# Optimization experiments

Measured on AMD Instinct MI355X. Metric: run time of the kernel, lower is better.

Reference implementation:

```python
import jax, jax.numpy as jnp
import numpy as np

B, D_IN, H = 4096, 1024, 2048
TAU_MIN = 0.2
ODE_STEPS = 3


def setup_inputs() -> dict:
    key = jax.random.key(0)
    ks = jax.random.split(key, 10)
    s = lambda k, shape, fan_in: jax.random.normal(k, shape, jnp.float32) / np.sqrt(fan_in)
    return {
        "x": jax.random.normal(ks[0], (B, D_IN), jnp.float32),
        "h": jax.random.normal(ks[1], (B, H), jnp.float32),
        "W_ih": s(ks[2], (H, D_IN), D_IN),
        "b_ih": jnp.zeros((H,), jnp.float32),
        "W_hh": s(ks[3], (H, H), H),
        "b_hh": jnp.zeros((H,), jnp.float32),
        "W_t1": s(ks[4], (H, D_IN + H), D_IN + H),
        "b_t1": jnp.zeros((H,), jnp.float32),
        "W_t2": s(ks[5], (H, H), H),
        "b_t2": jnp.zeros((H,), jnp.float32),
    }


def reference(x, h, W_ih, b_ih, W_hh, b_hh, W_t1, b_t1, W_t2, b_t2):
    # Precompute input-side projections (constant across ODE steps).
    ih = x @ W_ih.T + b_ih  # [B, H]

    def dynamics(h_cur):
        interaction = jnp.tanh(ih + h_cur @ W_hh.T + b_hh)
        z = jnp.concatenate([x, h_cur], axis=-1)  # [B, D_in+H]
        t1 = jax.nn.silu(z @ W_t1.T + b_t1)
        tau = jax.nn.softplus(t1 @ W_t2.T + b_t2) + TAU_MIN
        return (-h_cur + interaction) / tau

    dt = 1.0 / ODE_STEPS
    h_cur = h
    for _ in range(ODE_STEPS):  # RK2 (midpoint) steps
        k1 = dynamics(h_cur)
        h_mid = h_cur + 0.5 * dt * k1
        k2 = dynamics(h_mid)
        h_cur = h_cur + dt * k2
    return h_cur
```

## Files before the change

kernel.cpp:

```cpp
#include <hip/hip_runtime.h>


typedef _Float16 f16;
typedef __attribute__((ext_vector_type(4))) _Float16 f16x4;
typedef __attribute__((ext_vector_type(8))) _Float16 f16x8;
typedef __attribute__((ext_vector_type(4))) float f32x4;

#define TAU_MIN_F 0.2f

__device__ __forceinline__ float rcp_fast(float x) { return __builtin_amdgcn_rcpf(x); }
__device__ __forceinline__ float tanh_fast(float u) {
  float t = __expf(2.0f * u);
  return 1.0f - 2.0f * rcp_fast(t + 1.0f);
}
__device__ __forceinline__ float silu_fast(float u) {
  return u * rcp_fast(1.0f + __expf(-u));
}
__device__ __forceinline__ float softplus_fast(float u) {
  return fmaxf(u, 0.0f) + __logf(1.0f + __expf(-fabsf(u)));
}

__device__ __forceinline__ void glds16(const void* g, void* l) {
  __builtin_amdgcn_global_load_lds(
      (const __attribute__((address_space(1))) unsigned int*)g,
      (__attribute__((address_space(3))) unsigned int*)l,
      16, 0, 0);
}

__global__ void cvt4(const float* __restrict__ s, f16* __restrict__ d, int n4) {
  int i = blockIdx.x * 256 + threadIdx.x;
  if (i >= n4) return;
  float4 v = reinterpret_cast<const float4*>(s)[i];
  f16x4 o = {(_Float16)v.x, (_Float16)v.y, (_Float16)v.z, (_Float16)v.w};
  reinterpret_cast<f16x4*>(d)[i] = o;
}

__global__ void split_wt1(const float* __restrict__ Wt1, f16* __restrict__ Wpre,
                          f16* __restrict__ Wab) {
  int i = blockIdx.x * 256 + threadIdx.x;
  if (i >= 2048 * 768) return;
  int r = i / 768;
  int c4 = (i - r * 768) * 4;
  float4 v = reinterpret_cast<const float4*>(Wt1)[i];
  f16x4 o = {(_Float16)v.x, (_Float16)v.y, (_Float16)v.z, (_Float16)v.w};
  if (c4 < 1024)
    *reinterpret_cast<f16x4*>(Wpre + (size_t)(2048 + r) * 1024 + c4) = o;
  else
    *reinterpret_cast<f16x4*>(Wab + (size_t)(2048 + r) * 2048 + (c4 - 1024)) = o;
}

__global__ void biasprep(const float* __restrict__ bih, const float* __restrict__ bhh,
                         const float* __restrict__ bt1, float* __restrict__ biasp) {
  int i = blockIdx.x * 256 + threadIdx.x;
  if (i >= 4096) return;
  biasp[i] = (i < 2048) ? (bih[i] + bhh[i]) : bt1[i - 2048];
}

__global__ void init_h(const float* __restrict__ h, f16* __restrict__ hb,
                       float* __restrict__ hout) {
  int i = blockIdx.x * 256 + threadIdx.x;
  if (i >= 4096 * 2048 / 4) return;
  float4 v = reinterpret_cast<const float4*>(h)[i];
  reinterpret_cast<float4*>(hout)[i] = v;
  f16x4 o = {(_Float16)v.x, (_Float16)v.y, (_Float16)v.z, (_Float16)v.w};
  reinterpret_cast<f16x4*>(hb)[i] = o;
}

struct EpArgs {
  const float* biasf;
  const f16* pre16;
  const f16* h16;
  f16* out_d;
  f16* out_h;
  const float* bt2;
  const f16* diff;
  const float* h_base;
  float* out_f;
  float coef;
};

template <int EP>
__global__ __launch_bounds__(512, 2)
void gemm256(const f16* __restrict__ A, const f16* __restrict__ Bw,
             int N, int K, EpArgs ep) {
  __shared__ __align__(16) f16 SH[49152];

  const int gx = gridDim.x;
  const int nwg = gx * gridDim.y;
  const int orig = blockIdx.y * gx + blockIdx.x;
  const int cpx = nwg >> 3;
  const int w = (orig & 7) * cpx + (orig >> 3);
  const int bm = (w % gx) * 256;
  const int bn = (w / gx) * 256;

  const int tid = threadIdx.x;
  const int lane = tid & 63;
  const int wid = tid >> 6;
  const int wr = wid >> 2;
  const int wc = wid & 3;

  char* SHb = (char*)SH;

  const int srow = wid * 16 + (lane >> 2);
  const int skof = ((lane & 3) ^ ((lane >> 2) & 3)) << 4;
  const char* Ag0 = (const char*)A + (size_t)(bm + srow) * K * 2 + skof;
  const char* Ag1 = Ag0 + (size_t)128 * K * 2;
  const char* Bg0 = (const char*)Bw + (size_t)(bn + srow) * K * 2 + skof;
  const char* Bg1 = Bg0 + (size_t)128 * K * 2;
  const int dst = wid * 1024;

  const int fr = lane & 15;
  const int rxor = ((lane >> 4) ^ (fr & 3)) << 4;
  const int abase = (wr * 128 + fr) * 64 + rxor;
  const int bbase = 16384 + (wc * 64 + fr) * 64 + rxor;

  f32x4 acc[8][4] = {};
  const int NT = K >> 5;

  auto STAGE_A = [&](int t, int b) {
    const size_t kby = (size_t)t * 64;
    char* base = SHb + b * 32768;
    glds16(Ag0 + kby, base + dst);
    glds16(Ag1 + kby, base + 8192 + dst);
  };
  auto STAGE_B = [&](int t, int b) {
    const size_t kby = (size_t)t * 64;
    char* base = SHb + b * 32768;
    glds16(Bg0 + kby, base + 16384 + dst);
    glds16(Bg1 + kby, base + 24576 + dst);
  };

  STAGE_A(0, 0); STAGE_B(0, 0);
  STAGE_A(1, 1); STAGE_B(1, 1);

  int b = 0;
  for (int t = 0; t < NT - 1; ++t) {
    const int b2 = (b == 0) ? 2 : b - 1;
    asm volatile("s_waitcnt vmcnt(4)" ::: "memory");
    __builtin_amdgcn_s_barrier();
    __builtin_amdgcn_sched_barrier(0);
    const char* bufp = SHb + b * 32768;
    f16x8 af[4], bf[4];
#pragma unroll
    for (int i = 0; i < 4; ++i) af[i] = *reinterpret_cast<const f16x8*>(bufp + abase + i * 1024);
#pragma unroll
    for (int i = 0; i < 4; ++i) bf[i] = *reinterpret_cast<const f16x8*>(bufp + bbase + i * 1024);
    if (t + 2 < NT) STAGE_A(t + 2, b2);
    __builtin_amdgcn_s_barrier();
    __builtin_amdgcn_sched_barrier(0);
    asm volatile("s_waitcnt lgkmcnt(0)" ::: "memory");
    __builtin_amdgcn_sched_barrier(0);
    __builtin_amdgcn_s_setprio(1);
#pragma unroll
    for (int mi = 0; mi < 4; ++mi)
#pragma unroll
      for (int ni = 0; ni < 4; ++ni)
        acc[mi][ni] = __builtin_amdgcn_mfma_f32_16x16x32_f16(af[mi], bf[ni], acc[mi][ni], 0, 0, 0);
    __builtin_amdgcn_s_setprio(0);
    f16x8 ag[4];
#pragma unroll
    for (int i = 0; i < 4; ++i) ag[i] = *reinterpret_cast<const f16x8*>(bufp + abase + (4 + i) * 1024);
    if (t + 2 < NT) STAGE_B(t + 2, b2);
    __builtin_amdgcn_s_barrier();
    __builtin_amdgcn_sched_barrier(0);
    asm volatile("s_waitcnt lgkmcnt(0)" ::: "memory");
    __builtin_amdgcn_sched_barrier(0);
    __builtin_amdgcn_s_setprio(1);
#pragma unroll
    for (int mi = 0; mi < 4; ++mi)
#pragma unroll
      for (int ni = 0; ni < 4; ++ni)
        acc[4 + mi][ni] = __builtin_amdgcn_mfma_f32_16x16x32_f16(ag[mi], bf[ni], acc[4 + mi][ni], 0, 0, 0);
    __builtin_amdgcn_s_setprio(0);
    b = (b == 2) ? 0 : b + 1;
  }
  {
    asm volatile("s_waitcnt vmcnt(0)" ::: "memory");
    __builtin_amdgcn_s_barrier();
    __builtin_amdgcn_sched_barrier(0);
    const char* bufp = SHb + b * 32768;
    f16x8 af[4], bf[4];
#pragma unroll
    for (int i = 0; i < 4; ++i) af[i] = *reinterpret_cast<const f16x8*>(bufp + abase + i * 1024);
#pragma unroll
    for (int i = 0; i < 4; ++i) bf[i] = *reinterpret_cast<const f16x8*>(bufp + bbase + i * 1024);
#pragma unroll
    for (int mi = 0; mi < 4; ++mi)
#pragma unroll
      for (int ni = 0; ni < 4; ++ni)
        acc[mi][ni] = __builtin_amdgcn_mfma_f32_16x16x32_f16(af[mi], bf[ni], acc[mi][ni], 0, 0, 0);
    f16x8 ag[4];
#pragma unroll
    for (int i = 0; i < 4; ++i) ag[i] = *reinterpret_cast<const f16x8*>(bufp + abase + (4 + i) * 1024);
#pragma unroll
    for (int mi = 0; mi < 4; ++mi)
#pragma unroll
      for (int ni = 0; ni < 4; ++ni)
        acc[4 + mi][ni] = __builtin_amdgcn_mfma_f32_16x16x32_f16(ag[mi], bf[ni], acc[4 + mi][ni], 0, 0, 0);
  }
  __syncthreads();

  f16* tb = SH + wid * 1088;
  const int er = (lane >> 4) * 4;
  const int ec = lane & 15;
  const int rr = lane >> 3;
  const int cc = (lane & 7) * 8;
  const int colbase = bn + wc * 64;

#pragma unroll
  for (int mi = 0; mi < 8; ++mi) {
#pragma unroll
    for (int ni = 0; ni < 4; ++ni)
#pragma unroll
      for (int j = 0; j < 4; ++j)
        tb[(er + j) * 68 + ni * 16 + ec] = (f16)acc[mi][ni][j];
#pragma unroll
    for (int it = 0; it < 2; ++it) {
      const int row = rr + it * 8;
      const int gm = bm + wr * 128 + mi * 16 + row;
      const int gn = colbase + cc;
      f16x8 v = *reinterpret_cast<const f16x8*>(tb + row * 68 + cc);
      if constexpr (EP == 0) {
        float4 b0 = *reinterpret_cast<const float4*>(ep.biasf + gn);
        float4 b1 = *reinterpret_cast<const float4*>(ep.biasf + gn + 4);
        f16x8 o;
        o[0] = (f16)((float)v[0] + b0.x); o[1] = (f16)((float)v[1] + b0.y);
        o[2] = (f16)((float)v[2] + b0.z); o[3] = (f16)((float)v[3] + b0.w);
        o[4] = (f16)((float)v[4] + b1.x); o[5] = (f16)((float)v[5] + b1.y);
        o[6] = (f16)((float)v[6] + b1.z); o[7] = (f16)((float)v[7] + b1.w);
        *reinterpret_cast<f16x8*>(ep.out_h + (size_t)gm * N + gn) = o;
      } else {
        f16x8 pr = *reinterpret_cast<const f16x8*>(ep.pre16 + (size_t)gm * 4096 + gn);
        if (colbase < 2048) {
          f16x8 hh = *reinterpret_cast<const f16x8*>(ep.h16 + (size_t)gm * 2048 + gn);
          f16x8 o;
#pragma unroll
          for (int k = 0; k < 8; ++k) {
            float u = (float)v[k] + (float)pr[k];
            o[k] = (f16)(tanh_fast(u) - (float)hh[k]);
          }
          *reinterpret_cast<f16x8*>(ep.out_d + (size_t)gm * 2048 + gn) = o;
        } else {
          f16x8 o;
#pragma unroll
          for (int k = 0; k < 8; ++k) {
            float u = (float)v[k] + (float)pr[k];
            o[k] = (f16)silu_fast(u);
          }
          *reinterpret_cast<f16x8*>(ep.out_h + (size_t)gm * 2048 + (gn - 2048)) = o;
        }
      }
    }
  }
}

template <int EP>
__global__ __launch_bounds__(256)
void gemm_bt(const f16* __restrict__ A, const f16* __restrict__ Bw,
             int M, int N, int K, EpArgs ep) {
  __shared__ __align__(16) f16 SH[8192];

  const int gx = gridDim.x;
  const int nwg = gx * gridDim.y;
  const int orig = blockIdx.y * gx + blockIdx.x;
  const int cpx = nwg >> 3;
  const int w = (orig & 7) * cpx + (orig >> 3);
  const int bm = (w % gx) * 128;
  const int bn = (w / gx) * 128;

  const int tid = threadIdx.x;
  const int lane = tid & 63;
  const int wid = tid >> 6;
  const int wm = (wid >> 1) * 64;
  const int wn = (wid & 1) * 64;

  char* Asb = (char*)SH;
  char* Bsb = (char*)(SH + 4096);

  const int off0 = wid * 2048 + lane * 16;
  const int off1 = off0 + 1024;
  const int row0 = off0 >> 6, cb0 = off0 & 63;
  const int row1 = off1 >> 6, cb1 = off1 & 63;
  const char* Ag0 = (const char*)(A + (size_t)(bm + row0) * K) + cb0;
  const char* Ag1 = (const char*)(A + (size_t)(bm + row1) * K) + cb1;
  const char* Bg0 = (const char*)(Bw + (size_t)(bn + row0) * K) + cb0;
  const char* Bg1 = (const char*)(Bw + (size_t)(bn + row1) * K) + cb1;
  char* ldsA0 = Asb + wid * 2048;
  char* ldsA1 = Asb + wid * 2048 + 1024;
  char* ldsB0 = Bsb + wid * 2048;
  char* ldsB1 = Bsb + wid * 2048 + 1024;

  const int fr = lane & 15;
  const int kb = (lane >> 4) * 16;
  int aoff[4], boff[4];
#pragma unroll
  for (int i = 0; i < 4; ++i) {
    aoff[i] = (wm + i * 16 + fr) * 64 + kb;
    boff[i] = (wn + i * 16 + fr) * 64 + kb;
  }

  f32x4 acc[4][4] = {};
  const int nk = K >> 5;
  for (int kt = 0; kt < nk; ++kt) {
    const size_t kby = (size_t)kt * 64;
    glds16(Ag0 + kby, ldsA0);
    glds16(Ag1 + kby, ldsA1);
    glds16(Bg0 + kby, ldsB0);
    glds16(Bg1 + kby, ldsB1);
    __syncthreads();

    f16x8 af[4], bf[4];
#pragma unroll
    for (int i = 0; i < 4; ++i) af[i] = *reinterpret_cast<const f16x8*>(Asb + aoff[i]);
#pragma unroll
    for (int i = 0; i < 4; ++i) bf[i] = *reinterpret_cast<const f16x8*>(Bsb + boff[i]);

#pragma unroll
    for (int mi = 0; mi < 4; ++mi)
#pragma unroll
      for (int ni = 0; ni < 4; ++ni)
        acc[mi][ni] = __builtin_amdgcn_mfma_f32_16x16x32_f16(af[mi], bf[ni], acc[mi][ni], 0, 0, 0);

    __syncthreads();
  }

  f16* tb = SH + wid * 1088;
  const int er = (lane >> 4) * 4;
  const int ec = lane & 15;
  const int rr = lane >> 3;
  const int cc = (lane & 7) * 8;
  const int colbase = bn + wn;

#pragma unroll
  for (int mi = 0; mi < 4; ++mi) {
#pragma unroll
    for (int ni = 0; ni < 4; ++ni)
#pragma unroll
      for (int j = 0; j < 4; ++j)
        tb[(er + j) * 68 + ni * 16 + ec] = (f16)acc[mi][ni][j];
#pragma unroll
    for (int it = 0; it < 2; ++it) {
      const int row = rr + it * 8;
      const int gm = bm + wm + mi * 16 + row;
      const int gn = colbase + cc;
      f16x8 v = *reinterpret_cast<const f16x8*>(tb + row * 68 + cc);
      const size_t idx = (size_t)gm * 2048 + gn;
      float4 b0 = *reinterpret_cast<const float4*>(ep.bt2 + gn);
      float4 b1 = *reinterpret_cast<const float4*>(ep.bt2 + gn + 4);
      f16x8 df = *reinterpret_cast<const f16x8*>(ep.diff + idx);
      float4 h0 = *reinterpret_cast<const float4*>(ep.h_base + idx);
      float4 h1 = *reinterpret_cast<const float4*>(ep.h_base + idx + 4);
      float bb[8] = {b0.x, b0.y, b0.z, b0.w, b1.x, b1.y, b1.z, b1.w};
      float hb8[8] = {h0.x, h0.y, h0.z, h0.w, h1.x, h1.y, h1.z, h1.w};
      f16x8 o16;
      float on[8];
#pragma unroll
      for (int k = 0; k < 8; ++k) {
        float u = (float)v[k] + bb[k];
        float tau = softplus_fast(u) + TAU_MIN_F;
        float hn = hb8[k] + ep.coef * ((float)df[k] * rcp_fast(tau));
        on[k] = hn;
        o16[k] = (f16)hn;
      }
      *reinterpret_cast<f16x8*>(ep.out_h + idx) = o16;
      if (ep.out_f) {
        float4 o0 = {on[0], on[1], on[2], on[3]};
        float4 o1 = {on[4], on[5], on[6], on[7]};
        *reinterpret_cast<float4*>(ep.out_f + idx) = o0;
        *reinterpret_cast<float4*>(ep.out_f + idx + 4) = o1;
      }
    }
  }
}

extern "C" void kernel_launch(void* const* d_in, const int* in_sizes, int n_in,
                              void* d_out, int out_size, void* d_ws, size_t ws_size,
                              hipStream_t stream) {
  const float* x   = (const float*)d_in[0];
  const float* h   = (const float*)d_in[1];
  const float* Wih = (const float*)d_in[2];
  const float* bih = (const float*)d_in[3];
  const float* Whh = (const float*)d_in[4];
  const float* bhh = (const float*)d_in[5];
  const float* Wt1 = (const float*)d_in[6];
  const float* bt1 = (const float*)d_in[7];
  const float* Wt2 = (const float*)d_in[8];
  const float* bt2 = (const float*)d_in[9];
  float* hout = (float*)d_out;

  char* p = (char*)d_ws;
  auto alloc = [&](size_t bytes) {
    char* r = p;
    p += (bytes + 255) & ~(size_t)255;
    return r;
  };
  f16* xb    = (f16*)alloc((size_t)4096 * 1024 * 2);
  f16* Wpre  = (f16*)alloc((size_t)4096 * 1024 * 2);
  f16* Wab   = (f16*)alloc((size_t)4096 * 2048 * 2);
  f16* Wt2b  = (f16*)alloc((size_t)2048 * 2048 * 2);
  f16* hb    = (f16*)alloc((size_t)4096 * 2048 * 2);
  f16* hmb   = (f16*)alloc((size_t)4096 * 2048 * 2);
  f16* t1b   = (f16*)alloc((size_t)4096 * 2048 * 2);
  f16* pre16 = (f16*)alloc((size_t)4096 * 4096 * 2);
  f16* dif16 = (f16*)alloc((size_t)4096 * 2048 * 2);
  float* biasp = (float*)alloc(4096 * 4);

  cvt4<<<(4096 * 1024 / 4 + 255) / 256, 256, 0, stream>>>(x, xb, 4096 * 1024 / 4);
  cvt4<<<(2048 * 1024 / 4 + 255) / 256, 256, 0, stream>>>(Wih, Wpre, 2048 * 1024 / 4);
  cvt4<<<(2048 * 2048 / 4 + 255) / 256, 256, 0, stream>>>(Whh, Wab, 2048 * 2048 / 4);
  cvt4<<<(2048 * 2048 / 4 + 255) / 256, 256, 0, stream>>>(Wt2, Wt2b, 2048 * 2048 / 4);
  split_wt1<<<(2048 * 768 + 255) / 256, 256, 0, stream>>>(Wt1, Wpre, Wab);
  biasprep<<<16, 256, 0, stream>>>(bih, bhh, bt1, biasp);
  init_h<<<(4096 * 2048 / 4) / 256, 256, 0, stream>>>(h, hb, hout);

  {
    EpArgs e{};
    e.biasf = biasp;
    e.out_h = pre16;
    gemm256<0><<<dim3(16, 16), 512, 0, stream>>>(xb, Wpre, 4096, 1024, e);
  }

  const float dt = 1.0f / 3.0f;
  for (int s = 0; s < 3; ++s) {
    {
      EpArgs e{};
      e.pre16 = pre16; e.h16 = hb; e.out_d = dif16; e.out_h = t1b;
      gemm256<1><<<dim3(16, 16), 512, 0, stream>>>(hb, Wab, 4096, 2048, e);
    }
    {
      EpArgs e{};
      e.bt2 = bt2; e.diff = dif16; e.h_base = hout;
      e.coef = 0.5f * dt; e.out_f = nullptr; e.out_h = hmb;
      gemm_bt<2><<<dim3(32, 16), 256, 0, stream>>>(t1b, Wt2b, 4096, 2048, 2048, e);
    }
    {
      EpArgs e{};
      e.pre16 = pre16; e.h16 = hmb; e.out_d = dif16; e.out_h = t1b;
      gemm256<1><<<dim3(16, 16), 512, 0, stream>>>(hmb, Wab, 4096, 2048, e);
    }
    {
      EpArgs e{};
      e.bt2 = bt2; e.diff = dif16; e.h_base = hout;
      e.coef = dt; e.out_f = hout; e.out_h = hb;
      gemm_bt<2><<<dim3(32, 16), 256, 0, stream>>>(t1b, Wt2b, 4096, 2048, 2048, e);
    }
  }
}
```

Baseline: 945.3 us.

## Replace simple second-GEMM with pipelined 256x128 kernel and fuse prep kernels

```diff
diff --git a/kernel.cpp b/kernel.cpp
--- a/kernel.cpp
+++ b/kernel.cpp
@@ -27,43 +27,64 @@
       16, 0, 0);
 }
 
-__global__ void cvt4(const float* __restrict__ s, f16* __restrict__ d, int n4) {
-  int i = blockIdx.x * 256 + threadIdx.x;
-  if (i >= n4) return;
+__device__ __forceinline__ void cvt_one(const float* __restrict__ s,
+                                        f16* __restrict__ d, int i) {
   float4 v = reinterpret_cast<const float4*>(s)[i];
   f16x4 o = {(_Float16)v.x, (_Float16)v.y, (_Float16)v.z, (_Float16)v.w};
   reinterpret_cast<f16x4*>(d)[i] = o;
 }
 
-__global__ void split_wt1(const float* __restrict__ Wt1, f16* __restrict__ Wpre,
-                          f16* __restrict__ Wab) {
-  int i = blockIdx.x * 256 + threadIdx.x;
-  if (i >= 2048 * 768) return;
-  int r = i / 768;
-  int c4 = (i - r * 768) * 4;
-  float4 v = reinterpret_cast<const float4*>(Wt1)[i];
-  f16x4 o = {(_Float16)v.x, (_Float16)v.y, (_Float16)v.z, (_Float16)v.w};
-  if (c4 < 1024)
-    *reinterpret_cast<f16x4*>(Wpre + (size_t)(2048 + r) * 1024 + c4) = o;
-  else
-    *reinterpret_cast<f16x4*>(Wab + (size_t)(2048 + r) * 2048 + (c4 - 1024)) = o;
-}
-
-__global__ void biasprep(const float* __restrict__ bih, const float* __restrict__ bhh,
-                         const float* __restrict__ bt1, float* __restrict__ biasp) {
-  int i = blockIdx.x * 256 + threadIdx.x;
-  if (i >= 4096) return;
-  biasp[i] = (i < 2048) ? (bih[i] + bhh[i]) : bt1[i - 2048];
-}
-
-__global__ void init_h(const float* __restrict__ h, f16* __restrict__ hb,
-                       float* __restrict__ hout) {
-  int i = blockIdx.x * 256 + threadIdx.x;
-  if (i >= 4096 * 2048 / 4) return;
-  float4 v = reinterpret_cast<const float4*>(h)[i];
-  reinterpret_cast<float4*>(hout)[i] = v;
-  f16x4 o = {(_Float16)v.x, (_Float16)v.y, (_Float16)v.z, (_Float16)v.w};
-  reinterpret_cast<f16x4*>(hb)[i] = o;
+__global__ __launch_bounds__(256)
+void prep_all(const float* __restrict__ x, const float* __restrict__ h,
+              const float* __restrict__ Wih, const float* __restrict__ Whh,
+              const float* __restrict__ Wt1, const float* __restrict__ Wt2,
+              const float* __restrict__ bih, const float* __restrict__ bhh,
+              const float* __restrict__ bt1,
+              f16* __restrict__ xb, f16* __restrict__ hb,
+              f16* __restrict__ Wpre, f16* __restrict__ Wab,
+              f16* __restrict__ Wt2b, float* __restrict__ biasp) {
+  const int E0 = 1048576;
+  const int E1 = E0 + 524288;
+  const int E2 = E1 + 1048576;
+  const int E3 = E2 + 1048576;
+  const int E4 = E3 + 2097152;
+  const int E5 = E4 + 1572864;
+  const int E6 = E5 + 1024;
+  const int stride = gridDim.x * 256;
+  for (int i = blockIdx.x * 256 + threadIdx.x; i < E6; i += stride) {
+    if (i < E0) {
+      cvt_one(x, xb, i);
+    } else if (i < E1) {
+      cvt_one(Wih, Wpre, i - E0);
+    } else if (i < E2) {
+      cvt_one(Whh, Wab, i - E1);
+    } else if (i < E3) {
+      cvt_one(Wt2, Wt2b, i - E2);
+    } else if (i < E4) {
+      cvt_one(h, hb, i - E3);
+    } else if (i < E5) {
+      int j = i - E4;
+      int r = j / 768;
+      int c4 = (j - r * 768) * 4;
+      float4 v = reinterpret_cast<const float4*>(Wt1)[j];
+      f16x4 o = {(_Float16)v.x, (_Float16)v.y, (_Float16)v.z, (_Float16)v.w};
+      if (c4 < 1024)
+        *reinterpret_cast<f16x4*>(Wpre + (size_t)(2048 + r) * 1024 + c4) = o;
+      else
+        *reinterpret_cast<f16x4*>(Wab + (size_t)(2048 + r) * 2048 + (c4 - 1024)) = o;
+    } else {
+      int k = (i - E5) * 4;
+      float4 o;
+      if (k < 2048) {
+        float4 a = *reinterpret_cast<const float4*>(bih + k);
+        float4 bv = *reinterpret_cast<const float4*>(bhh + k);
+        o = {a.x + bv.x, a.y + bv.y, a.z + bv.z, a.w + bv.w};
+      } else {
+        o = *reinterpret_cast<const float4*>(bt1 + (k - 2048));
+      }
+      *reinterpret_cast<float4*>(biasp + k) = o;
+    }
+  }
 }
 
 struct EpArgs {
@@ -74,16 +95,17 @@
   f16* out_h;
   const float* bt2;
   const f16* diff;
-  const float* h_base;
+  const f16* hb16;
   float* out_f;
   float coef;
 };
 
 template <int EP>
 __global__ __launch_bounds__(512, 2)
-void gemm256(const f16* __restrict__ A, const f16* __restrict__ Bw,
-             int N, int K, EpArgs ep) {
-  __shared__ __align__(16) f16 SH[49152];
+void gemmT(const f16* __restrict__ A, const f16* __restrict__ Bw,
+           int N, int K, EpArgs ep) {
+  constexpr int BUFB = 32768;
+  __shared__ __align__(16) char SH[BUFB * 3];
 
   const int gx = gridDim.x;
   const int nwg = gx * gridDim.y;
@@ -99,8 +121,6 @@
   const int wr = wid >> 2;
   const int wc = wid & 3;
 
-  char* SHb = (char*)SH;
-
   const int srow = wid * 16 + (lane >> 2);
   const int skof = ((lane & 3) ^ ((lane >> 2) & 3)) << 4;
   const char* Ag0 = (const char*)A + (size_t)(bm + srow) * K * 2 + skof;
@@ -119,13 +139,13 @@
 
   auto STAGE_A = [&](int t, int b) {
     const size_t kby = (size_t)t * 64;
-    char* base = SHb + b * 32768;
+    char* base = SH + b * BUFB;
     glds16(Ag0 + kby, base + dst);
     glds16(Ag1 + kby, base + 8192 + dst);
   };
   auto STAGE_B = [&](int t, int b) {
     const size_t kby = (size_t)t * 64;
-    char* base = SHb + b * 32768;
+    char* base = SH + b * BUFB;
     glds16(Bg0 + kby, base + 16384 + dst);
     glds16(Bg1 + kby, base + 24576 + dst);
   };
@@ -139,7 +159,7 @@
     asm volatile("s_waitcnt vmcnt(4)" ::: "memory");
     __builtin_amdgcn_s_barrier();
     __builtin_amdgcn_sched_barrier(0);
-    const char* bufp = SHb + b * 32768;
+    const char* bufp = SH + b * BUFB;
     f16x8 af[4], bf[4];
 #pragma unroll
     for (int i = 0; i < 4; ++i) af[i] = *reinterpret_cast<const f16x8*>(bufp + abase + i * 1024);
@@ -170,7 +190,8 @@
     for (int mi = 0; mi < 4; ++mi)
 #pragma unroll
       for (int ni = 0; ni < 4; ++ni)
-        acc[4 + mi][ni] = __builtin_amdgcn_mfma_f32_16x16x32_f16(ag[mi], bf[ni], acc[4 + mi][ni], 0, 0, 0);
+        acc[4 + mi][ni] =
+            __builtin_amdgcn_mfma_f32_16x16x32_f16(ag[mi], bf[ni], acc[4 + mi][ni], 0, 0, 0);
     __builtin_amdgcn_s_setprio(0);
     b = (b == 2) ? 0 : b + 1;
   }
@@ -178,7 +199,7 @@
     asm volatile("s_waitcnt vmcnt(0)" ::: "memory");
     __builtin_amdgcn_s_barrier();
     __builtin_amdgcn_sched_barrier(0);
-    const char* bufp = SHb + b * 32768;
+    const char* bufp = SH + b * BUFB;
     f16x8 af[4], bf[4];
 #pragma unroll
     for (int i = 0; i < 4; ++i) af[i] = *reinterpret_cast<const f16x8*>(bufp + abase + i * 1024);
@@ -196,11 +217,12 @@
     for (int mi = 0; mi < 4; ++mi)
 #pragma unroll
       for (int ni = 0; ni < 4; ++ni)
-        acc[4 + mi][ni] = __builtin_amdgcn_mfma_f32_16x16x32_f16(ag[mi], bf[ni], acc[4 + mi][ni], 0, 0, 0);
+        acc[4 + mi][ni] =
+            __builtin_amdgcn_mfma_f32_16x16x32_f16(ag[mi], bf[ni], acc[4 + mi][ni], 0, 0, 0);
   }
   __syncthreads();
 
-  f16* tb = SH + wid * 1088;
+  f16* tb = (f16*)SH + wid * 1088;
   const int er = (lane >> 4) * 4;
   const int ec = lane & 15;
   const int rr = lane >> 3;
@@ -254,121 +276,135 @@
   }
 }
 
-template <int EP>
-__global__ __launch_bounds__(256)
-void gemm_bt(const f16* __restrict__ A, const f16* __restrict__ Bw,
-             int M, int N, int K, EpArgs ep) {
-  __shared__ __align__(16) f16 SH[8192];
+__global__ __launch_bounds__(512, 2)
+void gemmC(const f16* __restrict__ A, const f16* __restrict__ Bw,
+           int K, EpArgs ep) {
+  constexpr int BUFB = 24576;
+  __shared__ __align__(16) char SH[BUFB * 3];
 
   const int gx = gridDim.x;
   const int nwg = gx * gridDim.y;
   const int orig = blockIdx.y * gx + blockIdx.x;
   const int cpx = nwg >> 3;
   const int w = (orig & 7) * cpx + (orig >> 3);
-  const int bm = (w % gx) * 128;
+  const int bm = (w % gx) * 256;
   const int bn = (w / gx) * 128;
 
   const int tid = threadIdx.x;
   const int lane = tid & 63;
   const int wid = tid >> 6;
-  const int wm = (wid >> 1) * 64;
-  const int wn = (wid & 1) * 64;
-
-  char* Asb = (char*)SH;
-  char* Bsb = (char*)(SH + 4096);
-
-  const int off0 = wid * 2048 + lane * 16;
-  const int off1 = off0 + 1024;
-  const int row0 = off0 >> 6, cb0 = off0 & 63;
-  const int row1 = off1 >> 6, cb1 = off1 & 63;
-  const char* Ag0 = (const char*)(A + (size_t)(bm + row0) * K) + cb0;
-  const char* Ag1 = (const char*)(A + (size_t)(bm + row1) * K) + cb1;
-  const char* Bg0 = (const char*)(Bw + (size_t)(bn + row0) * K) + cb0;
-  const char* Bg1 = (const char*)(Bw + (size_t)(bn + row1) * K) + cb1;
-  char* ldsA0 = Asb + wid * 2048;
-  char* ldsA1 = Asb + wid * 2048 + 1024;
-  char* ldsB0 = Bsb + wid * 2048;
-  char* ldsB1 = Bsb + wid * 2048 + 1024;
+  const int wr = wid >> 2;
+  const int wc = wid & 3;
+
+  const int srow = wid * 16 + (lane >> 2);
+  const int skof = ((lane & 3) ^ ((lane >> 2) & 3)) << 4;
+  const char* Ag0 = (const char*)A + (size_t)(bm + srow) * K * 2 + skof;
+  const char* Ag1 = Ag0 + (size_t)128 * K * 2;
+  const char* Bg0 = (const char*)Bw + (size_t)(bn + srow) * K * 2 + skof;
+  const int dst = wid * 1024;
 
   const int fr = lane & 15;
-  const int kb = (lane >> 4) * 16;
-  int aoff[4], boff[4];
-#pragma unroll
-  for (int i = 0; i < 4; ++i) {
-    aoff[i] = (wm + i * 16 + fr) * 64 + kb;
-    boff[i] = (wn + i * 16 + fr) * 64 + kb;
-  }
-
-  f32x4 acc[4][4] = {};
-  const int nk = K >> 5;
-  for (int kt = 0; kt < nk; ++kt) {
-    const size_t kby = (size_t)kt * 64;
-    glds16(Ag0 + kby, ldsA0);
-    glds16(Ag1 + kby, ldsA1);
-    glds16(Bg0 + kby, ldsB0);
-    glds16(Bg1 + kby, ldsB1);
-    __syncthreads();
-
-    f16x8 af[4], bf[4];
-#pragma unroll
-    for (int i = 0; i < 4; ++i) af[i] = *reinterpret_cast<const f16x8*>(Asb + aoff[i]);
-#pragma unroll
-    for (int i = 0; i < 4; ++i) bf[i] = *reinterpret_cast<const f16x8*>(Bsb + boff[i]);
-
-#pragma unroll
-    for (int mi = 0; mi < 4; ++mi)
-#pragma unroll
-      for (int ni = 0; ni < 4; ++ni)
+  const int rxor = ((lane >> 4) ^ (fr & 3)) << 4;
+  const int abase = (wr * 128 + fr) * 64 + rxor;
+  const int bbase = 16384 + (wc * 32 + fr) * 64 + rxor;
+
+  f32x4 acc[8][2] = {};
+  const int NT = K >> 5;
+
+  auto STAGE = [&](int t, int b) {
+    const size_t kby = (size_t)t * 64;
+    char* base = SH + b * BUFB;
+    glds16(Ag0 + kby, base + dst);
+    glds16(Ag1 + kby, base + 8192 + dst);
+    glds16(Bg0 + kby, base + 16384 + dst);
+  };
+
+  STAGE(0, 0); STAGE(1, 1);
+
+  int b = 0;
+  for (int t = 0; t < NT - 1; ++t) {
+    const int b2 = (b == 0) ? 2 : b - 1;
+    asm volatile("s_waitcnt vmcnt(3)" ::: "memory");
+    __builtin_amdgcn_s_barrier();
+    __builtin_amdgcn_sched_barrier(0);
+    const char* bufp = SH + b * BUFB;
+    f16x8 af[8], bf[2];
+#pragma unroll
+    for (int i = 0; i < 8; ++i) af[i] = *reinterpret_cast<const f16x8*>(bufp + abase + i * 1024);
+#pragma unroll
+    for (int i = 0; i < 2; ++i) bf[i] = *reinterpret_cast<const f16x8*>(bufp + bbase + i * 1024);
+    if (t + 2 < NT) STAGE(t + 2, b2);
+    __builtin_amdgcn_s_barrier();
+    __builtin_amdgcn_sched_barrier(0);
+    asm volatile("s_waitcnt lgkmcnt(0)" ::: "memory");
+    __builtin_amdgcn_sched_barrier(0);
+    __builtin_amdgcn_s_setprio(1);
+#pragma unroll
+    for (int mi = 0; mi < 8; ++mi)
+#pragma unroll
+      for (int ni = 0; ni < 2; ++ni)
         acc[mi][ni] = __builtin_amdgcn_mfma_f32_16x16x32_f16(af[mi], bf[ni], acc[mi][ni], 0, 0, 0);
-
-    __syncthreads();
-  }
-
-  f16* tb = SH + wid * 1088;
+    __builtin_amdgcn_s_setprio(0);
+    b = (b == 2) ? 0 : b + 1;
+  }
+  {
+    asm volatile("s_waitcnt vmcnt(0)" ::: "memory");
+    __builtin_amdgcn_s_barrier();
+    __builtin_amdgcn_sched_barrier(0);
+    const char* bufp = SH + b * BUFB;
+    f16x8 af[8], bf[2];
+#pragma unroll
+    for (int i = 0; i < 8; ++i) af[i] = *reinterpret_cast<const f16x8*>(bufp + abase + i * 1024);
+#pragma unroll
+    for (int i = 0; i < 2; ++i) bf[i] = *reinterpret_cast<const f16x8*>(bufp + bbase + i * 1024);
+#pragma unroll
+    for (int mi = 0; mi < 8; ++mi)
+#pragma unroll
+      for (int ni = 0; ni < 2; ++ni)
+        acc[mi][ni] = __builtin_amdgcn_mfma_f32_16x16x32_f16(af[mi], bf[ni], acc[mi][ni], 0, 0, 0);
+  }
+  __syncthreads();
+
+  f16* tb = (f16*)SH + wid * 576;
   const int er = (lane >> 4) * 4;
   const int ec = lane & 15;
-  const int rr = lane >> 3;
-  const int cc = (lane & 7) * 8;
-  const int colbase = bn + wn;
-
-#pragma unroll
-  for (int mi = 0; mi < 4; ++mi) {
-#pragma unroll
-    for (int ni = 0; ni < 4; ++ni)
+  const int rr = lane >> 2;
+  const int cc = (lane & 3) * 8;
+  const int colbase = bn + wc * 32;
+
+#pragma unroll
+  for (int mi = 0; mi < 8; ++mi) {
+#pragma unroll
+    for (int ni = 0; ni < 2; ++ni)
 #pragma unroll
       for (int j = 0; j < 4; ++j)
-        tb[(er + j) * 68 + ni * 16 + ec] = (f16)acc[mi][ni][j];
-#pragma unroll
-    for (int it = 0; it < 2; ++it) {
-      const int row = rr + it * 8;
-      const int gm = bm + wm + mi * 16 + row;
-      const int gn = colbase + cc;
-      f16x8 v = *reinterpret_cast<const f16x8*>(tb + row * 68 + cc);
-      const size_t idx = (size_t)gm * 2048 + gn;
-      float4 b0 = *reinterpret_cast<const float4*>(ep.bt2 + gn);
-      float4 b1 = *reinterpret_cast<const float4*>(ep.bt2 + gn + 4);
-      f16x8 df = *reinterpret_cast<const f16x8*>(ep.diff + idx);
-      float4 h0 = *reinterpret_cast<const float4*>(ep.h_base + idx);
-      float4 h1 = *reinterpret_cast<const float4*>(ep.h_base + idx + 4);
-      float bb[8] = {b0.x, b0.y, b0.z, b0.w, b1.x, b1.y, b1.z, b1.w};
-      float hb8[8] = {h0.x, h0.y, h0.z, h0.w, h1.x, h1.y, h1.z, h1.w};
-      f16x8 o16;
-      float on[8];
-#pragma unroll
-      for (int k = 0; k < 8; ++k) {
-        float u = (float)v[k] + bb[k];
-        float tau = softplus_fast(u) + TAU_MIN_F;
-        float hn = hb8[k] + ep.coef * ((float)df[k] * rcp_fast(tau));
-        on[k] = hn;
-        o16[k] = (f16)hn;
-      }
-      *reinterpret_cast<f16x8*>(ep.out_h + idx) = o16;
-      if (ep.out_f) {
-        float4 o0 = {on[0], on[1], on[2], on[3]};
-        float4 o1 = {on[4], on[5], on[6], on[7]};
-        *reinterpret_cast<float4*>(ep.out_f + idx) = o0;
-        *reinterpret_cast<float4*>(ep.out_f + idx + 4) = o1;
-      }
+        tb[(er + j) * 36 + ni * 16 + ec] = (f16)acc[mi][ni][j];
+    const int row = rr;
+    const int gm = bm + wr * 128 + mi * 16 + row;
+    const int gn = colbase + cc;
+    f16x8 v = *reinterpret_cast<const f16x8*>(tb + row * 36 + cc);
+    const size_t idx = (size_t)gm * 2048 + gn;
+    float4 b0 = *reinterpret_cast<const float4*>(ep.bt2 + gn);
+    float4 b1 = *reinterpret_cast<const float4*>(ep.bt2 + gn + 4);
+    f16x8 df = *reinterpret_cast<const f16x8*>(ep.diff + idx);
+    f16x8 hbv = *reinterpret_cast<const f16x8*>(ep.hb16 + idx);
+    float bb[8] = {b0.x, b0.y, b0.z, b0.w, b1.x, b1.y, b1.z, b1.w};
+    f16x8 o16;
+    float on[8];
+#pragma unroll
+    for (int k = 0; k < 8; ++k) {
+      float u = (float)v[k] + bb[k];
+      float tau = softplus_fast(u) + TAU_MIN_F;
+      float hn = (float)hbv[k] + ep.coef * ((float)df[k] * rcp_fast(tau));
+      on[k] = hn;
+      o16[k] = (f16)hn;
+    }
+    *reinterpret_cast<f16x8*>(ep.out_h + idx) = o16;
+    if (ep.out_f) {
+      float4 o0 = {on[0], on[1], on[2], on[3]};
+      float4 o1 = {on[4], on[5], on[6], on[7]};
+      *reinterpret_cast<float4*>(ep.out_f + idx) = o0;
+      *reinterpret_cast<float4*>(ep.out_f + idx + 4) = o1;
     }
   }
 }
@@ -405,19 +441,14 @@
   f16* dif16 = (f16*)alloc((size_t)4096 * 2048 * 2);
   float* biasp = (float*)alloc(4096 * 4);
 
-  cvt4<<<(4096 * 1024 / 4 + 255) / 256, 256, 0, stream>>>(x, xb, 4096 * 1024 / 4);
-  cvt4<<<(2048 * 1024 / 4 + 255) / 256, 256, 0, stream>>>(Wih, Wpre, 2048 * 1024 / 4);
-  cvt4<<<(2048 * 2048 / 4 + 255) / 256, 256, 0, stream>>>(Whh, Wab, 2048 * 2048 / 4);
-  cvt4<<<(2048 * 2048 / 4 + 255) / 256, 256, 0, stream>>>(Wt2, Wt2b, 2048 * 2048 / 4);
-  split_wt1<<<(2048 * 768 + 255) / 256, 256, 0, stream>>>(Wt1, Wpre, Wab);
-  biasprep<<<16, 256, 0, stream>>>(bih, bhh, bt1, biasp);
-  init_h<<<(4096 * 2048 / 4) / 256, 256, 0, stream>>>(h, hb, hout);
+  prep_all<<<2048, 256, 0, stream>>>(x, h, Wih, Whh, Wt1, Wt2, bih, bhh, bt1,
+                                     xb, hb, Wpre, Wab, Wt2b, biasp);
 
   {
     EpArgs e{};
     e.biasf = biasp;
     e.out_h = pre16;
-    gemm256<0><<<dim3(16, 16), 512, 0, stream>>>(xb, Wpre, 4096, 1024, e);
+    gemmT<0><<<dim3(16, 16), 512, 0, stream>>>(xb, Wpre, 4096, 1024, e);
   }
 
   const float dt = 1.0f / 3.0f;
@@ -425,24 +456,24 @@
     {
       EpArgs e{};
       e.pre16 = pre16; e.h16 = hb; e.out_d = dif16; e.out_h = t1b;
-      gemm256<1><<<dim3(16, 16), 512, 0, stream>>>(hb, Wab, 4096, 2048, e);
+      gemmT<1><<<dim3(16, 16), 512, 0, stream>>>(hb, Wab, 4096, 2048, e);
     }
     {
       EpArgs e{};
-      e.bt2 = bt2; e.diff = dif16; e.h_base = hout;
-      e.coef = 0.5f * dt; e.out_f = nullptr; e.out_h = hmb;
-      gemm_bt<2><<<dim3(32, 16), 256, 0, stream>>>(t1b, Wt2b, 4096, 2048, 2048, e);
+      e.bt2 = bt2; e.diff = dif16; e.hb16 = hb;
+      e.coef = 0.5f * dt / 1.0f; e.out_f = nullptr; e.out_h = hmb;
+      gemmC<<<dim3(16, 16), 512, 0, stream>>>(t1b, Wt2b, 2048, e);
     }
     {
       EpArgs e{};
       e.pre16 = pre16; e.h16 = hmb; e.out_d = dif16; e.out_h = t1b;
-      gemm256<1><<<dim3(16, 16), 512, 0, stream>>>(hmb, Wab, 4096, 2048, e);
+      gemmT<1><<<dim3(16, 16), 512, 0, stream>>>(hmb, Wab, 4096, 2048, e);
     }
     {
       EpArgs e{};
-      e.bt2 = bt2; e.diff = dif16; e.h_base = hout;
-      e.coef = dt; e.out_f = hout; e.out_h = hb;
-      gemm_bt<2><<<dim3(32, 16), 256, 0, stream>>>(t1b, Wt2b, 4096, 2048, 2048, e);
-    }
-  }
-}
+      e.bt2 = bt2; e.diff = dif16; e.hb16 = hb;
+      e.coef = dt; e.out_f = (s == 2) ? hout : nullptr; e.out_h = hb;
+      gemmC<<<dim3(16, 16), 512, 0, stream>>>(t1b, Wt2b, 2048, e);
+    }
+  }
+}
```

New measurement: 844.4 us. -10.7%, faster.
